# Kernel optimization log

Measured on AMD Instinct MI355X. Metric: run time of the kernel, lower is better.

## Reference

```python
import jax, jax.numpy as jnp
import numpy as np

K = 5          # kernel_size per dim
B = 100        # batch size (hard-coded in source)
GRID = 28
NUM_FIRST_FC = 49  # adjs[2].size(0) = 7*7


def spline_conv(x, edge_index, pseudo, W, root, bias):
    """Degree-1 open B-spline graph conv (SplineGCN).
    x: [N, Cin]; edge_index: [2, E] (src, dst); pseudo: [E, 2] in [0,1];
    W: [K*K, Cin, Cout]; root: [Cin, Cout]; bias: [Cout].
    out_i = mean_{j->i} sum_taps b_tap(u_ij) * (x_j @ W[k_tap]) + x_i @ root + bias
    """
    N = x.shape[0]
    src, dst = edge_index[0], edge_index[1]
    pos = pseudo * (K - 1)                     # open spline: scale to [0, K-1]
    kf = jnp.floor(pos)
    frac = pos - kf                            # [E, 2]
    k0 = kf.astype(jnp.int32)
    k1 = jnp.minimum(k0 + 1, K - 1)
    # Precompute x @ W[k] for all 25 kernel indices: [N, K*K, Cout]
    y = jnp.einsum('ni,kio->nko', x, W)
    fx, fy = frac[:, 0], frac[:, 1]
    taps = [
        (k0[:, 0], k0[:, 1], (1 - fx) * (1 - fy)),
        (k0[:, 0], k1[:, 1], (1 - fx) * fy),
        (k1[:, 0], k0[:, 1], fx * (1 - fy)),
        (k1[:, 0], k1[:, 1], fx * fy),
    ]
    msg = jnp.zeros((src.shape[0], W.shape[2]), dtype=x.dtype)
    for ax, ay, w in taps:
        msg = msg + w[:, None] * y[src, ax * K + ay]   # gather [E, Cout]
    agg = jax.ops.segment_sum(msg, dst, num_segments=N)
    deg = jax.ops.segment_sum(jnp.ones_like(msg[:, 0]), dst, num_segments=N)
    return agg / jnp.maximum(deg, 1.0)[:, None] + x @ root + bias


def max_pool2(x):  # x: [b, H, W, C] -> [b, H/2, W/2, C] (same math as NCHW pool)
    b, h, w, c = x.shape
    return x.reshape(b, h // 2, 2, w // 2, 2, c).max(axis=(2, 4))


def setup_inputs() -> dict:
    key = jax.random.key(0)
    ks = jax.random.split(key, 16)
    N0, N1 = B * GRID * GRID, B * (GRID // 2) * (GRID // 2)
    E0, E1 = N0 * 8, N1 * 8
    s = 0.1
    return {
        'x': jax.random.normal(ks[0], (N0, 1), dtype=jnp.float32),
        'pseudo0': jax.random.uniform(ks[1], (E0, 2), dtype=jnp.float32),
        'pseudo1': jax.random.uniform(ks[2], (E1, 2), dtype=jnp.float32),
        'W1': jax.random.normal(ks[3], (K * K, 1, 32), dtype=jnp.float32) * s,
        'root1': jax.random.normal(ks[4], (1, 32), dtype=jnp.float32) * s,
        'b1': jnp.zeros((32,), dtype=jnp.float32),
        'W2': jax.random.normal(ks[5], (K * K, 32, 64), dtype=jnp.float32) * s,
        'root2': jax.random.normal(ks[6], (32, 64), dtype=jnp.float32) * s,
        'b2': jnp.zeros((64,), dtype=jnp.float32),
        'fc1_w': jax.random.normal(ks[7], (NUM_FIRST_FC * 64, 512), dtype=jnp.float32) * 0.02,
        'fc1_b': jnp.zeros((512,), dtype=jnp.float32),
        'fc2_w': jax.random.normal(ks[8], (512, 10), dtype=jnp.float32) * 0.02,
        'fc2_b': jnp.zeros((10,), dtype=jnp.float32),
        'edge_index0': jax.random.randint(ks[9], (2, E0), 0, N0, dtype=jnp.int32),
        'edge_index1': jax.random.randint(ks[10], (2, E1), 0, N1, dtype=jnp.int32),
    }


def reference(x, pseudo0, pseudo1, W1, root1, b1, W2, root2, b2,
              fc1_w, fc1_b, fc2_w, fc2_b, edge_index0, edge_index1):
    elu = jax.nn.elu
    # conv1 on 28x28 grid graph
    h = elu(spline_conv(x, edge_index0, pseudo0, W1, root1, b1))   # [B*784, 32]
    h = h.reshape(-1, GRID, GRID, 32)                              # [B, 28, 28, 32]
    h = max_pool2(h)                                               # [B, 14, 14, 32]
    h = h.reshape(-1, 32)                                          # [B*196, 32]
    # conv2 on 14x14 grid graph
    h = elu(spline_conv(h, edge_index1, pseudo1, W2, root2, b2))   # [B*196, 64]
    # faithful replication of the source's reshapes: (B*196) rows -> (B/4, 28, 28, 64)
    h = h.reshape(-1, GRID, GRID, 64)                              # [25, 28, 28, 64]
    h = max_pool2(h)                                               # [25, 14, 14, 64]
    h = h.reshape(-1, NUM_FIRST_FC * 64)                           # [100, 3136]
    h = elu(h @ fc1_w + fc1_b)
    # F.dropout with training=False (eval) is identity
    h = elu(h @ fc2_w + fc2_b)
    return jax.nn.log_softmax(h, axis=-1)
```

## Files before the change

### kernel.cpp

```cpp
#include <hip/hip_runtime.h>
#include <hip/hip_bf16.h>

#define KK 5
constexpr int N0 = 78400;
constexpr int E0 = 627200;
constexpr int N1 = 19600;
constexpr int E1 = 156800;
constexpr int C1 = 32, C2 = 64;
constexpr int BSZ = 100;
constexpr int FC1_IN = 3136, FC1_OUT = 512;
constexpr int NKEYS = 98000;
constexpr int NCOARSE = 383;
constexpr int CAPB = 2400;
constexpr int KEXT = 832;
constexpr int ULS = 836;
constexpr int UBS = 856;
constexpr int CH2 = 160;
constexpr int CH1 = 640;

typedef __attribute__((ext_vector_type(8))) short bf16x8;
typedef __attribute__((ext_vector_type(4))) float f32x4;

__device__ __forceinline__ unsigned short f2bf(float f) {
    union { float f; unsigned u; } v; v.f = f;
    unsigned u = v.u;
    unsigned r = (u + 0x7FFF + ((u >> 16) & 1)) >> 16;
    return (unsigned short)r;
}

__device__ __forceinline__ void taps4(float px, float py,
                                      int& a00, int& a01, int& a10, int& a11,
                                      float& fx, float& fy) {
    float kfx = floorf(px), kfy = floorf(py);
    fx = px - kfx; fy = py - kfy;
    int k0x = min(max((int)kfx, 0), KK - 1);
    int k0y = min(max((int)kfy, 0), KK - 1);
    int k1x = min(k0x + 1, KK - 1), k1y = min(k0y + 1, KK - 1);
    a00 = k0x * KK + k0y; a01 = k0x * KK + k1y;
    a10 = k1x * KK + k0y; a11 = k1x * KK + k1y;
}

__global__ void coarse_bin(const int* __restrict__ ei0, const int* __restrict__ ei1,
                           int* __restrict__ gcur, int* __restrict__ pk) {
    __shared__ int hist[NCOARSE];
    __shared__ int gbase[NCOARSE];
    int t = threadIdx.x;
    for (int i = t; i < NCOARSE; i += 512) hist[i] = 0;
    __syncthreads();
    int e0b = blockIdx.x * 4096;
    int ids[8], keys[8], rnk[8];
#pragma unroll
    for (int j = 0; j < 8; j++) {
        int e = e0b + t + j * 512;
        int gk = -1, id = 0;
        if (e < E0) { gk = ei0[E0 + e]; id = e; }
        else if (e < E0 + E1) { int el = e - E0; gk = N0 + ei1[E1 + el]; id = el; }
        ids[j] = id; keys[j] = gk;
    }
#pragma unroll
    for (int j = 0; j < 8; j++)
        if (keys[j] >= 0) rnk[j] = atomicAdd(&hist[keys[j] >> 8], 1);
    __syncthreads();
    for (int i = t; i < NCOARSE; i += 512)
        gbase[i] = hist[i] ? atomicAdd(&gcur[i], hist[i]) : 0;
    __syncthreads();
#pragma unroll
    for (int j = 0; j < 8; j++) {
        if (keys[j] >= 0) {
            int b = keys[j] >> 8;
            int p = gbase[b] + rnk[j];
            if (p < CAPB) pk[b * CAPB + p] = ids[j] | ((keys[j] & 255) << 20);
        }
    }
}

__global__ void tiny_scan(const int* __restrict__ gcur, int* __restrict__ db,
                          int* __restrict__ off) {
    __shared__ int tmp[NCOARSE];
    int t = threadIdx.x;
    if (t < NCOARSE) tmp[t] = min(gcur[t], CAPB);
    __syncthreads();
    if (t == 0) {
        int s = 0;
        for (int i = 0; i < NCOARSE; i++) { int c = tmp[i]; tmp[i] = s; s += c; }
    }
    __syncthreads();
    if (t < NCOARSE) db[t] = tmp[t];
    if (t == 0) off[NKEYS] = E0 + E1;
}

__global__ void fine_sort(const int* __restrict__ pk, const int* __restrict__ gcur,
                          const int* __restrict__ db,
                          int* __restrict__ idxx, int* __restrict__ off) {
    __shared__ int ent[CAPB];
    __shared__ int rnk[CAPB];
    __shared__ int h2[256];
    __shared__ int sc[256];
    int b = blockIdx.x, t = threadIdx.x;
    int cb = min(gcur[b], CAPB);
    int base = db[b];
    h2[t] = 0;
    __syncthreads();
    for (int i = t; i < cb; i += 256) {
        int v = pk[b * CAPB + i];
        ent[i] = v;
        rnk[i] = atomicAdd(&h2[(v >> 20) & 255], 1);
    }
    __syncthreads();
    int v0 = h2[t];
    sc[t] = v0;
    __syncthreads();
    for (int d = 1; d < 256; d <<= 1) {
        int add = (t >= d) ? sc[t - d] : 0;
        __syncthreads();
        sc[t] += add;
        __syncthreads();
    }
    int excl = sc[t] - v0;
    __syncthreads();
    sc[t] = excl;
    __syncthreads();
    int n = (b << 8) + t;
    if (n < NKEYS) off[n] = base + excl;
    for (int i = t; i < cb; i += 256) {
        int v = ent[i];
        idxx[base + sc[(v >> 20) & 255] + rnk[i]] = v & 0xFFFFF;
    }
}

__global__ __launch_bounds__(256, 4)
void conv1_pool(const int* __restrict__ idxx, const int* __restrict__ off,
                const float* __restrict__ x, const int* __restrict__ ei0,
                const float* __restrict__ ps0, const float* __restrict__ W1,
                const float* __restrict__ root, const float* __restrict__ bias,
                float* __restrict__ p1) {
    __shared__ float S4[224 * 25];
    __shared__ float Sr[56 * 25];
    __shared__ float exv[CH1], efx[CH1], efy[CH1];
    __shared__ int   emt[CH1];
    float* h1t = S4;
    int t = threadIdx.x;
    int bb = blockIdx.x;
    int n0 = bb * 56;
    int q = t & 3, nl = t >> 2;
    bool actN = nl < 56;
    int n = n0 + (actN ? nl : 0);
    float* sp = S4 + (actN ? (nl * 4 + q) : 0) * 25;
    for (int i = t; i < 224 * 25; i += 256) S4[i] = 0.f;
    int e0 = off[n0], e1 = off[n0 + 56];
    int my0 = off[n], my1 = off[n + 1];
    for (int base = e0; base < e1; base += CH1) {
        int nE = min(e1 - base, CH1);
        __syncthreads();
        for (int j = t; j < nE; j += 256) {
            int e = idxx[base + j];
            int src = ei0[e];
            int a00, a01, a10, a11; float fx, fy;
            taps4(ps0[2 * e] * (KK - 1), ps0[2 * e + 1] * (KK - 1),
                  a00, a01, a10, a11, fx, fy);
            emt[j] = a00 | (a01 << 5) | (a10 << 10) | (a11 << 15);
            efx[j] = fx; efy[j] = fy;
            exv[j] = x[src];
        }
        __syncthreads();
        if (actN) {
            int r0 = max(my0 - base, 0), r1 = min(my1 - base, nE);
            for (int p = r0 + q; p < r1; p += 4) {
                float xv = exv[p]; int m = emt[p];
                float fx = efx[p], fy = efy[p];
                float gx = 1.f - fx, gy = 1.f - fy;
                sp[m & 31]         += gx * gy * xv;
                sp[(m >> 5) & 31]  += gx * fy * xv;
                sp[(m >> 10) & 31] += fx * gy * xv;
                sp[(m >> 15) & 31] += fx * fy * xv;
            }
        }
    }
    __syncthreads();
    for (int i2 = t; i2 < 56 * 25; i2 += 256) {
        int n2 = i2 / 25, a = i2 - n2 * 25;
        Sr[i2] = S4[(n2 * 4 + 0) * 25 + a] + S4[(n2 * 4 + 1) * 25 + a] +
                 S4[(n2 * 4 + 2) * 25 + a] + S4[(n2 * 4 + 3) * 25 + a];
    }
    __syncthreads();
    {
        int o = t & 31, ng = t >> 5;
        float w1c[25];
#pragma unroll
        for (int a = 0; a < 25; a++) w1c[a] = W1[a * C1 + o];
        float ro = root[o], bo = bias[o];
        for (int j2 = 0; j2 < 7; j2++) {
            int nl2 = ng * 7 + j2;
            int n2 = n0 + nl2;
            float acc = 0.f;
#pragma unroll
            for (int a = 0; a < 25; a++) acc += Sr[nl2 * 25 + a] * w1c[a];
            float invd = 1.f / fmaxf((float)(off[n2 + 1] - off[n2]), 1.f);
            float v = acc * invd + x[n2] * ro + bo;
            h1t[nl2 * 32 + o] = v > 0.f ? v : expm1f(v);
        }
    }
    __syncthreads();
    for (int i2 = t; i2 < 448; i2 += 256) {
        int o2 = i2 & 31, pc = i2 >> 5;
        float m0 = h1t[(2 * pc) * 32 + o2],      m1 = h1t[(2 * pc + 1) * 32 + o2];
        float m2 = h1t[(28 + 2 * pc) * 32 + o2], m3 = h1t[(28 + 2 * pc + 1) * 32 + o2];
        p1[(bb * 14 + pc) * C1 + o2] = fmaxf(fmaxf(m0, m1), fmaxf(m2, m3));
    }
}

__global__ void prep_weights(const float* __restrict__ w, const float* __restrict__ W2,
                             const float* __restrict__ root2,
                             unsigned short* __restrict__ wt1,
                             unsigned short* __restrict__ w2t) {
    if (blockIdx.x == 49) {
        int base = blockIdx.y * 6656;
        for (int i = threadIdx.x; i < 6656; i += 256) {
            int idx = base + i;
            int o = idx / KEXT, k = idx - o * KEXT;
            float v = (k < 800) ? W2[k * 64 + o] : root2[(k - 800) * 64 + o];
            w2t[idx] = f2bf(v);
        }
        return;
    }
    __shared__ unsigned short tile[64 * 66];
    int t = threadIdx.x;
    int k0 = blockIdx.x * 64, j0 = blockIdx.y * 64;
    int jj = t & 63, ks = t >> 6;
    for (int kk = ks; kk < 64; kk += 4)
        tile[kk * 66 + jj] = f2bf(w[(k0 + kk) * FC1_OUT + j0 + jj]);
    __syncthreads();
    int kk = t & 63, js = t >> 6;
    for (int j2 = js; j2 < 64; j2 += 4)
        wt1[(j0 + j2) * FC1_IN + k0 + kk] = tile[kk * 66 + j2];
}

__global__ __launch_bounds__(256, 5)
void conv2_fused(const float* __restrict__ p1, const int* __restrict__ idxx,
                 const int* __restrict__ off, const int* __restrict__ ei1,
                 const float* __restrict__ ps1,
                 const unsigned short* __restrict__ w2t,
                 const float* __restrict__ b2, float* __restrict__ h2) {
    __shared__ float Ul[8 * ULS];
    __shared__ int   es[CH2];
    __shared__ int   et[CH2];
    __shared__ float efx[CH2], efy[CH2];
    unsigned short* Ub = (unsigned short*)Ul;
    int t = threadIdx.x;
    int nb = blockIdx.x * 8;
    int i = t & 31, g = t >> 5;
    float* up = Ul + g * ULS;
#pragma unroll
    for (int a = 0; a < 25; a++) up[a * 32 + i] = 0.f;
    up[800 + i] = p1[(nb + g) * C1 + i];
    int e0 = off[N0 + nb], e1 = off[N0 + nb + 8];
    int my0 = off[N0 + nb + g], my1 = off[N0 + nb + g + 1];
    for (int base = e0; base < e1; base += CH2) {
        int nE = min(e1 - base, CH2);
        __syncthreads();
        for (int j = t; j < nE; j += 256) {
            int e = idxx[base + j];
            es[j] = ei1[e];
            int a00, a01, a10, a11; float fx, fy;
            taps4(ps1[2 * e] * (KK - 1), ps1[2 * e + 1] * (KK - 1),
                  a00, a01, a10, a11, fx, fy);
            et[j] = a00 | (a01 << 5) | (a10 << 10) | (a11 << 15);
            efx[j] = fx; efy[j] = fy;
        }
        __syncthreads();
        int r0 = max(my0 - base, 0);
        int r1 = min(my1 - base, nE);
        int myT = max(r1 - r0, 0);
        int m64 = max(myT, __shfl_xor(myT, 32));
#pragma unroll 2
        for (int jj = 0; jj < m64; jj++) {
            int j = r0 + jj;
            bool act = j < r1;
            int ji = act ? j : 0;
            int src = es[ji]; int m = et[ji];
            float fx = efx[ji], fy = efy[ji];
            float xv = p1[src * C1 + i];
            if (act) {
                float gx = 1.f - fx, gy = 1.f - fy;
                up[(m & 31) * 32 + i]         += gx * gy * xv;
                up[((m >> 5) & 31) * 32 + i]  += gx * fy * xv;
                up[((m >> 10) & 31) * 32 + i] += fx * gy * xv;
                up[((m >> 15) & 31) * 32 + i] += fx * fy * xv;
            }
        }
    }
    __syncthreads();
    {
        int g2 = t >> 5, ks = (t & 31) * 26;
        int dgc = off[N0 + nb + g2 + 1] - off[N0 + nb + g2];
        float invd = 1.f / fmaxf((float)dgc, 1.f);
        const float* srcp = Ul + g2 * ULS + ks;
        float rv[26];
#pragma unroll
        for (int j = 0; j < 26; j++) {
            float v = srcp[j];
            rv[j] = (ks + j < 800) ? v * invd : v;
        }
        __syncthreads();
        unsigned* dstp = (unsigned*)(Ub + g2 * UBS + ks);
#pragma unroll
        for (int j = 0; j < 13; j++) {
            unsigned lo = f2bf(rv[2 * j]), hi = f2bf(rv[2 * j + 1]);
            dstp[j] = lo | (hi << 16);
        }
    }
    __syncthreads();
    int wv = t >> 6, lane = t & 63, quad = lane >> 4, lrow = lane & 15;
    f32x4 acc = {0.f, 0.f, 0.f, 0.f};
    int nodeA = lrow & 7;
    const unsigned short* bbase = w2t + (wv * 16 + lrow) * KEXT;
    const unsigned short* abase = Ub + nodeA * UBS;
#pragma unroll
    for (int kc = 0; kc < 26; kc++) {
        bf16x8 a = *(const bf16x8*)(abase + kc * 32 + quad * 8);
        bf16x8 b = *(const bf16x8*)(bbase + kc * 32 + quad * 8);
        acc = __builtin_amdgcn_mfma_f32_16x16x32_bf16(a, b, acc, 0, 0, 0);
    }
    if (quad < 2) {
        int o = wv * 16 + lrow;
        float bo = b2[o];
#pragma unroll
        for (int r = 0; r < 4; r++) {
            int node = quad * 4 + r;
            float v = acc[r] + bo;
            v = v > 0.f ? v : expm1f(v);
            h2[(nb + node) * C2 + o] = v;
        }
    }
}

__global__ void pool2b(const float* __restrict__ h2, unsigned short* __restrict__ p2b) {
    int idx = blockIdx.x * blockDim.x + threadIdx.x;
    if (idx >= 112 * FC1_IN) return;
    if (idx >= 100 * FC1_IN) { p2b[idx] = 0; return; }
    int o = idx & 63; int t2 = idx >> 6;
    int c = t2 % 14; int r = (t2 / 14) % 14; int b = t2 / 196;
    const float* base = h2 + (((b * 28 + 2 * r) * 28 + 2 * c) * C2 + o);
    float m = fmaxf(fmaxf(base[0], base[C2]),
                    fmaxf(base[28 * C2], base[28 * C2 + C2]));
    p2b[idx] = f2bf(m);
}

__global__ void gemm_fc1(const unsigned short* __restrict__ p2b,
                         const unsigned short* __restrict__ wt1,
                         float* __restrict__ z1p) {
    constexpr int AS = 232;
    __shared__ unsigned short as_[16 * AS];
    int t = threadIdx.x;
    int jt = blockIdx.x, mt = blockIdx.y, kz = blockIdx.z;
    int wv = t >> 6, lane = t & 63, quad = lane >> 4, lrow = lane & 15;
    int m0 = mt * 16;
    int kbase = kz * 1568;
    const unsigned short* bbase = wt1 + (jt * 64 + wv * 16 + lrow) * FC1_IN + kbase;
    f32x4 acc = {0.f, 0.f, 0.f, 0.f};
    for (int ch = 0; ch < 7; ch++) {
        __syncthreads();
        for (int slot = t; slot < 448; slot += 256) {
            int r = slot / 28, c = slot - (slot / 28) * 28;
            *(uint4*)(as_ + r * AS + c * 8) =
                *(const uint4*)(p2b + (m0 + r) * FC1_IN + kbase + ch * 224 + c * 8);
        }
        __syncthreads();
        const unsigned short* ab = as_ + lrow * AS;
        const unsigned short* bb = bbase + ch * 224;
#pragma unroll
        for (int kk = 0; kk < 7; kk++) {
            bf16x8 a = *(const bf16x8*)(ab + kk * 32 + quad * 8);
            bf16x8 b = *(const bf16x8*)(bb + kk * 32 + quad * 8);
            acc = __builtin_amdgcn_mfma_f32_16x16x32_bf16(a, b, acc, 0, 0, 0);
        }
    }
    int n = jt * 64 + wv * 16 + lrow;
#pragma unroll
    for (int r = 0; r < 4; r++) {
        int m = m0 + quad * 4 + r;
        z1p[kz * (112 * FC1_OUT) + m * FC1_OUT + n] = acc[r];
    }
}

__global__ void fc2_lsm(const float* __restrict__ z1p, const float* __restrict__ fc1b,
                        const float* __restrict__ w, const float* __restrict__ fc2b,
                        float* __restrict__ out) {
    int b = blockIdx.x;
    int t = threadIdx.x;
    int wv = t >> 6;
    int lane = t & 63;
    float acc = 0.f;
#pragma unroll
    for (int m = 0; m < 8; m++) {
        int k = lane * 8 + m;
        float xv = fc1b[k] + z1p[b * FC1_OUT + k] + z1p[112 * FC1_OUT + b * FC1_OUT + k];
        xv = xv > 0.f ? xv : expm1f(xv);
        acc += xv * w[k * 10 + wv];
    }
#pragma unroll
    for (int off = 32; off > 0; off >>= 1) acc += __shfl_down(acc, off);
    __shared__ float zs[10];
    if (lane == 0) {
        float z = acc + fc2b[wv];
        zs[wv] = z > 0.f ? z : expm1f(z);
    }
    __syncthreads();
    if (t < 10) {
        float m = -1e30f;
        for (int jj = 0; jj < 10; jj++) m = fmaxf(m, zs[jj]);
        float s = 0.f;
        for (int jj = 0; jj < 10; jj++) s += expf(zs[jj] - m);
        out[b * 10 + t] = zs[t] - m - logf(s);
    }
}

extern "C" void kernel_launch(void* const* d_in, const int* in_sizes, int n_in,
                              void* d_out, int out_size, void* d_ws, size_t ws_size,
                              hipStream_t stream) {
    const float* x     = (const float*)d_in[0];
    const float* ps0   = (const float*)d_in[1];
    const float* ps1   = (const float*)d_in[2];
    const float* W1    = (const float*)d_in[3];
    const float* root1 = (const float*)d_in[4];
    const float* b1    = (const float*)d_in[5];
    const float* W2    = (const float*)d_in[6];
    const float* root2 = (const float*)d_in[7];
    const float* b2v   = (const float*)d_in[8];
    const float* fc1w  = (const float*)d_in[9];
    const float* fc1b  = (const float*)d_in[10];
    const float* fc2w  = (const float*)d_in[11];
    const float* fc2b  = (const float*)d_in[12];
    const int*   ei0   = (const int*)d_in[13];
    const int*   ei1   = (const int*)d_in[14];

    float* ws = (float*)d_ws;
    int* gcur  = (int*)ws;
    int* db    = (int*)(ws + 384);
    int* off   = (int*)(ws + 768);
    int* pk    = (int*)(ws + 98772);
    int* idxx  = (int*)(ws + 1017972);
    float* p1  = ws + 1801972;
    float* h2  = ws + 2429172;
    unsigned short* p2b = (unsigned short*)(ws + 3683572);
    float* z1p = ws + 3859188;
    unsigned short* w2t = (unsigned short*)(ws + 3973876);
    unsigned short* wt1 = (unsigned short*)(ws + 4000500);

    hipMemsetAsync(gcur, 0, (size_t)NCOARSE * sizeof(int), stream);

    coarse_bin<<<(E0 + E1 + 4095) / 4096, 512, 0, stream>>>(ei0, ei1, gcur, pk);
    tiny_scan<<<1, 512, 0, stream>>>(gcur, db, off);
    fine_sort<<<NCOARSE, 256, 0, stream>>>(pk, gcur, db, idxx, off);
    prep_weights<<<dim3(50, 8), 256, 0, stream>>>(fc1w, W2, root2, wt1, w2t);
    conv1_pool<<<1400, 256, 0, stream>>>(idxx, off, x, ei0, ps0,
                                         W1, root1, b1, p1);
    conv2_fused<<<N1 / 8, 256, 0, stream>>>(p1, idxx, off, ei1, ps1, w2t, b2v, h2);
    pool2b<<<(112 * FC1_IN + 255) / 256, 256, 0, stream>>>(h2, p2b);
    gemm_fc1<<<dim3(8, 7, 2), 256, 0, stream>>>(p2b, wt1, z1p);
    fc2_lsm<<<BSZ, 640, 0, stream>>>(z1p, fc1b, fc2w, fc2b, (float*)d_out);
}
```

Baseline: 228.0 us.

## Fold weight prep into binning kernel, fold scan into fine sort, unroll conv2 loop

Weight transposition and bf16 conversion now run as extra blocks of the coarse_bin kernel, so they overlap with edge binning. The single-block tiny_scan kernel is removed, and each fine_sort block computes its own base offset with a block reduction over the coarse counts. Together these remove two kernel launches and one serial step. The conv2 edge loop is also hand-unrolled by two to overlap the gathers, at the cost of redundant per-block reduction work and higher register use.

```diff
diff --git a/kernel.cpp b/kernel.cpp
--- a/kernel.cpp
+++ b/kernel.cpp
@@ -41,10 +41,37 @@
 }
 
 __global__ void coarse_bin(const int* __restrict__ ei0, const int* __restrict__ ei1,
-                           int* __restrict__ gcur, int* __restrict__ pk) {
+                           int* __restrict__ gcur, int* __restrict__ pk,
+                           const float* __restrict__ fc1w, const float* __restrict__ W2,
+                           const float* __restrict__ root2,
+                           unsigned short* __restrict__ wt1,
+                           unsigned short* __restrict__ w2t) {
     __shared__ int hist[NCOARSE];
     __shared__ int gbase[NCOARSE];
+    __shared__ unsigned short tile[64 * 66];
     int t = threadIdx.x;
+    if (blockIdx.x >= 192) {
+        int pb = blockIdx.x - 192;
+        if (pb >= 392) {
+            int base = (pb - 392) * 6656;
+            for (int i2 = t; i2 < 6656; i2 += 512) {
+                int idx = base + i2;
+                int o = idx / KEXT, k = idx - o * KEXT;
+                float v = (k < 800) ? W2[k * 64 + o] : root2[(k - 800) * 64 + o];
+                w2t[idx] = f2bf(v);
+            }
+            return;
+        }
+        int k0 = (pb >> 3) * 64, j0 = (pb & 7) * 64;
+        int jj = t & 63, ks = t >> 6;
+        for (int kk = ks; kk < 64; kk += 8)
+            tile[kk * 66 + jj] = f2bf(fc1w[(k0 + kk) * FC1_OUT + j0 + jj]);
+        __syncthreads();
+        int kk2 = t & 63, js = t >> 6;
+        for (int j2 = js; j2 < 64; j2 += 8)
+            wt1[(j0 + j2) * FC1_IN + k0 + kk2] = tile[kk2 * 66 + j2];
+        return;
+    }
     for (int i = t; i < NCOARSE; i += 512) hist[i] = 0;
     __syncthreads();
     int e0b = blockIdx.x * 4096;
@@ -74,31 +101,31 @@
     }
 }
 
-__global__ void tiny_scan(const int* __restrict__ gcur, int* __restrict__ db,
-                          int* __restrict__ off) {
-    __shared__ int tmp[NCOARSE];
-    int t = threadIdx.x;
-    if (t < NCOARSE) tmp[t] = min(gcur[t], CAPB);
-    __syncthreads();
-    if (t == 0) {
-        int s = 0;
-        for (int i = 0; i < NCOARSE; i++) { int c = tmp[i]; tmp[i] = s; s += c; }
-    }
-    __syncthreads();
-    if (t < NCOARSE) db[t] = tmp[t];
-    if (t == 0) off[NKEYS] = E0 + E1;
-}
-
 __global__ void fine_sort(const int* __restrict__ pk, const int* __restrict__ gcur,
-                          const int* __restrict__ db,
                           int* __restrict__ idxx, int* __restrict__ off) {
+    __shared__ int cl[NCOARSE];
     __shared__ int ent[CAPB];
     __shared__ int rnk[CAPB];
     __shared__ int h2[256];
     __shared__ int sc[256];
+    __shared__ int redbuf[4];
+    __shared__ int baseS;
     int b = blockIdx.x, t = threadIdx.x;
-    int cb = min(gcur[b], CAPB);
-    int base = db[b];
+    for (int i2 = t; i2 < NCOARSE; i2 += 256) cl[i2] = min(gcur[i2], CAPB);
+    __syncthreads();
+    {
+        int s = 0;
+        if (t < b) s += cl[t];
+        if (t + 256 < b) s += cl[t + 256];
+#pragma unroll
+        for (int o2 = 32; o2 > 0; o2 >>= 1) s += __shfl_down(s, o2);
+        if ((t & 63) == 0) redbuf[t >> 6] = s;
+        __syncthreads();
+        if (t == 0) baseS = redbuf[0] + redbuf[1] + redbuf[2] + redbuf[3];
+        __syncthreads();
+    }
+    int base = baseS;
+    int cb = cl[b];
     h2[t] = 0;
     __syncthreads();
     for (int i = t; i < cb; i += 256) {
@@ -122,6 +149,7 @@
     __syncthreads();
     int n = (b << 8) + t;
     if (n < NKEYS) off[n] = base + excl;
+    if (b == 0 && t == 0) off[NKEYS] = E0 + E1;
     for (int i = t; i < cb; i += 256) {
         int v = ent[i];
         idxx[base + sc[(v >> 20) & 255] + rnk[i]] = v & 0xFFFFF;
@@ -209,32 +237,6 @@
     }
 }
 
-__global__ void prep_weights(const float* __restrict__ w, const float* __restrict__ W2,
-                             const float* __restrict__ root2,
-                             unsigned short* __restrict__ wt1,
-                             unsigned short* __restrict__ w2t) {
-    if (blockIdx.x == 49) {
-        int base = blockIdx.y * 6656;
-        for (int i = threadIdx.x; i < 6656; i += 256) {
-            int idx = base + i;
-            int o = idx / KEXT, k = idx - o * KEXT;
-            float v = (k < 800) ? W2[k * 64 + o] : root2[(k - 800) * 64 + o];
-            w2t[idx] = f2bf(v);
-        }
-        return;
-    }
-    __shared__ unsigned short tile[64 * 66];
-    int t = threadIdx.x;
-    int k0 = blockIdx.x * 64, j0 = blockIdx.y * 64;
-    int jj = t & 63, ks = t >> 6;
-    for (int kk = ks; kk < 64; kk += 4)
-        tile[kk * 66 + jj] = f2bf(w[(k0 + kk) * FC1_OUT + j0 + jj]);
-    __syncthreads();
-    int kk = t & 63, js = t >> 6;
-    for (int j2 = js; j2 < 64; j2 += 4)
-        wt1[(j0 + j2) * FC1_IN + k0 + kk] = tile[kk * 66 + j2];
-}
-
 __global__ __launch_bounds__(256, 5)
 void conv2_fused(const float* __restrict__ p1, const int* __restrict__ idxx,
                  const int* __restrict__ off, const int* __restrict__ ei1,
@@ -272,20 +274,28 @@
         int r1 = min(my1 - base, nE);
         int myT = max(r1 - r0, 0);
         int m64 = max(myT, __shfl_xor(myT, 32));
-#pragma unroll 2
-        for (int jj = 0; jj < m64; jj++) {
-            int j = r0 + jj;
-            bool act = j < r1;
-            int ji = act ? j : 0;
-            int src = es[ji]; int m = et[ji];
-            float fx = efx[ji], fy = efy[ji];
-            float xv = p1[src * C1 + i];
-            if (act) {
-                float gx = 1.f - fx, gy = 1.f - fy;
-                up[(m & 31) * 32 + i]         += gx * gy * xv;
-                up[((m >> 5) & 31) * 32 + i]  += gx * fy * xv;
-                up[((m >> 10) & 31) * 32 + i] += fx * gy * xv;
-                up[((m >> 15) & 31) * 32 + i] += fx * fy * xv;
+        for (int jj = 0; jj < m64; jj += 2) {
+            bool a0 = jj < myT, a1 = jj + 1 < myT;
+            int j0 = a0 ? r0 + jj : 0, j1 = a1 ? r0 + jj + 1 : 0;
+            int s0 = es[j0], s1 = es[j1];
+            int mm0 = et[j0], mm1 = et[j1];
+            float fx0 = efx[j0], fy0 = efy[j0];
+            float fx1 = efx[j1], fy1 = efy[j1];
+            float x0 = p1[s0 * C1 + i];
+            float x1 = p1[s1 * C1 + i];
+            if (a0) {
+                float gx = 1.f - fx0, gy = 1.f - fy0;
+                up[(mm0 & 31) * 32 + i]         += gx * gy * x0;
+                up[((mm0 >> 5) & 31) * 32 + i]  += gx * fy0 * x0;
+                up[((mm0 >> 10) & 31) * 32 + i] += fx0 * gy * x0;
+                up[((mm0 >> 15) & 31) * 32 + i] += fx0 * fy0 * x0;
+            }
+            if (a1) {
+                float gx = 1.f - fx1, gy = 1.f - fy1;
+                up[(mm1 & 31) * 32 + i]         += gx * gy * x1;
+                up[((mm1 >> 5) & 31) * 32 + i]  += gx * fy1 * x1;
+                up[((mm1 >> 10) & 31) * 32 + i] += fx1 * gy * x1;
+                up[((mm1 >> 15) & 31) * 32 + i] += fx1 * fy1 * x1;
             }
         }
     }
@@ -436,23 +446,20 @@
 
     float* ws = (float*)d_ws;
     int* gcur  = (int*)ws;
-    int* db    = (int*)(ws + 384);
-    int* off   = (int*)(ws + 768);
-    int* pk    = (int*)(ws + 98772);
-    int* idxx  = (int*)(ws + 1017972);
-    float* p1  = ws + 1801972;
-    float* h2  = ws + 2429172;
-    unsigned short* p2b = (unsigned short*)(ws + 3683572);
-    float* z1p = ws + 3859188;
-    unsigned short* w2t = (unsigned short*)(ws + 3973876);
-    unsigned short* wt1 = (unsigned short*)(ws + 4000500);
+    int* off   = (int*)(ws + 384);
+    int* pk    = (int*)(ws + 98388);
+    int* idxx  = (int*)(ws + 1017588);
+    float* p1  = ws + 1801588;
+    float* h2  = ws + 2428788;
+    unsigned short* p2b = (unsigned short*)(ws + 3683188);
+    float* z1p = ws + 3858804;
+    unsigned short* w2t = (unsigned short*)(ws + 3973492);
+    unsigned short* wt1 = (unsigned short*)(ws + 4000116);
 
     hipMemsetAsync(gcur, 0, (size_t)NCOARSE * sizeof(int), stream);
 
-    coarse_bin<<<(E0 + E1 + 4095) / 4096, 512, 0, stream>>>(ei0, ei1, gcur, pk);
-    tiny_scan<<<1, 512, 0, stream>>>(gcur, db, off);
-    fine_sort<<<NCOARSE, 256, 0, stream>>>(pk, gcur, db, idxx, off);
-    prep_weights<<<dim3(50, 8), 256, 0, stream>>>(fc1w, W2, root2, wt1, w2t);
+    coarse_bin<<<592, 512, 0, stream>>>(ei0, ei1, gcur, pk, fc1w, W2, root2, wt1, w2t);
+    fine_sort<<<NCOARSE, 256, 0, stream>>>(pk, gcur, idxx, off);
     conv1_pool<<<1400, 256, 0, stream>>>(idxx, off, x, ei0, ps0,
                                          W1, root1, b1, p1);
     conv2_fused<<<N1 / 8, 256, 0, stream>>>(p1, idxx, off, ei1, ps1, w2t, b2v, h2);
```

Measured after the change: 218.7 us. -4.1%, faster.
